# Performance work log

Measured on AMD Instinct MI355X. Metric: run time of the kernel, lower is better.

Reference implementation:

```python
import jax, jax.numpy as jnp
import numpy as np


def _gru(xs, w_ih, w_hh, b_ih, b_hh):
    """Batch-first torch-style GRU. xs: (B,T,I) -> (B,T,H)."""
    b, t, _ = xs.shape
    H = w_hh.shape[1]
    xp = xs @ w_ih.T + b_ih  # (B,T,3H): precomputed input projections

    def step(h, xp_t):
        gh = h @ w_hh.T + b_hh  # (B,3H)
        xr, xz, xn = xp_t[:, :H], xp_t[:, H:2 * H], xp_t[:, 2 * H:]
        hr, hz, hn = gh[:, :H], gh[:, H:2 * H], gh[:, 2 * H:]
        r = jax.nn.sigmoid(xr + hr)
        z = jax.nn.sigmoid(xz + hz)
        n = jnp.tanh(xn + r * hn)
        h_new = (1.0 - z) * n + z * h
        return h_new, h_new

    h0 = jnp.zeros((b, H), dtype=xs.dtype)
    _, hs = jax.lax.scan(step, h0, jnp.swapaxes(xp, 0, 1))  # (T,B,H)
    return jnp.swapaxes(hs, 0, 1)


def reference(x, gru_w_ih, gru_w_hh, gru_b_ih, gru_b_hh, filter_alpha, pc_w, pc_b, pat_re, pat_im):
    b, t, _ = x.shape
    xs = x[..., 0]  # (B,T)
    # quaternionic lift: (w,x,y,z) = (s, .1s, .01s, .001s)
    quat = jnp.stack([xs, 0.1 * xs, 0.01 * xs, 0.001 * xs], axis=-1)  # (B,T,4)
    evolved = _gru(quat, gru_w_ih, gru_w_hh, gru_b_ih, gru_b_hh)  # (B,T,4*dim)
    dim2 = evolved.shape[-1] // 2
    ev = evolved.reshape(b, t, dim2, 2)
    ec = jax.lax.complex(ev[..., 0], ev[..., 1])  # (B,T,2*dim) complex64
    fd = jnp.fft.fft(ec, axis=1)
    kmag = jnp.abs(fd) + 1e-10
    pf = filter_alpha[0] * jnp.arctan(jnp.log(kmag))  # phase filter
    filtered = fd * jax.lax.complex(jnp.cos(pf), jnp.sin(pf))
    ft = jnp.fft.ifft(filtered, axis=1).real  # (B,T,2*dim) float32
    coh = ft.reshape(b, t, -1) @ pc_w.T + pc_b  # (B,T,dim)
    # interference logits: |<x_t, pattern_j>|^2, computed only for batch 0
    # (faithful to original; x_t is real so vdot conjugation is a no-op)
    x0 = coh[0]  # (T,dim)
    zr = x0 @ pat_re.T  # (T,V)
    zi = x0 @ pat_im.T  # (T,V)
    logits0 = zr * zr + zi * zi
    return logits0[None]  # (1,T,V)


def setup_inputs() -> dict:
    key = jax.random.key(0)
    ks = jax.random.split(key, 10)
    dim, T, V = 128, 4096, 32000
    H = dim * 4
    return {
        "x": jax.random.normal(ks[0], (1, T, 1), jnp.float32),
        "gru_w_ih": jax.random.normal(ks[1], (3 * H, 4), jnp.float32) * 0.05,
        "gru_w_hh": jax.random.normal(ks[2], (3 * H, H), jnp.float32) * 0.05,
        "gru_b_ih": jax.random.normal(ks[3], (3 * H,), jnp.float32) * 0.05,
        "gru_b_hh": jax.random.normal(ks[4], (3 * H,), jnp.float32) * 0.05,
        "filter_alpha": jnp.ones((1,), jnp.float32) * 1.5,
        "pc_w": jax.random.normal(ks[5], (dim, 2 * dim), jnp.float32) * 0.05,
        "pc_b": jax.random.normal(ks[6], (dim,), jnp.float32) * 0.05,
        "pat_re": jax.random.normal(ks[7], (V, dim), jnp.float32) * 0.1,
        "pat_im": jax.random.normal(ks[8], (V, dim), jnp.float32) * 0.1,
    }
```

## Files before the change

kernel.cpp:

```cpp
#include <hip/hip_runtime.h>

#define T_STEPS 4096
#define HID     512
#define NCH     256
#define DIM     128
#define VOCAB   32000
#define GRU_WGS 32

__global__ __launch_bounds__(256) void gru_kernel(
    const float* __restrict__ x,
    const float* __restrict__ w_ih,
    const float* __restrict__ w_hh,
    const float* __restrict__ b_ih,
    const float* __restrict__ b_hh,
    unsigned long long* hg,
    float* __restrict__ evolved)
{
  __shared__ float hs[HID];
  const int tid  = threadIdx.x;
  const int wave = tid >> 6;
  const int lane = tid & 63;
  const int team = lane >> 4;
  const int p    = lane & 15;
  const int pr   = p & 7;
  const int j    = blockIdx.x * 16 + wave * 4 + team;
  const int k0   = p * 32;

  float4 w[3][8];
#pragma unroll
  for (int d = 0; d < 3; ++d) {
    const float4* wr = reinterpret_cast<const float4*>(w_hh + (size_t)(d * HID + j) * HID);
#pragma unroll
    for (int qq = 0; qq < 8; ++qq) {
      const int r = (qq + pr) & 7;
      w[d][qq] = wr[p * 8 + r];
    }
  }
  float c3[3], bi3[3], bh3[3];
#pragma unroll
  for (int d = 0; d < 3; ++d) {
    int r = d * HID + j;
    c3[d]  = w_ih[r*4+0] + 0.1f*w_ih[r*4+1] + 0.01f*w_ih[r*4+2] + 0.001f*w_ih[r*4+3];
    bi3[d] = b_ih[r];
    bh3[d] = b_hh[r];
  }

  float hprev = 0.0f;
  for (int s = 1; s <= T_STEPS; ++s) {
    const int rb = (s - 1) & 1;
    const int wb = s & 1;
    const unsigned int want = (unsigned int)(s - 1);
    const unsigned long long* rs = hg + rb * HID;

    const float xt = x[s - 1];

    unsigned long long vA, vB;
    for (;;) {
      vA = __hip_atomic_load(rs + 2 * tid,     __ATOMIC_RELAXED, __HIP_MEMORY_SCOPE_AGENT);
      vB = __hip_atomic_load(rs + 2 * tid + 1, __ATOMIC_RELAXED, __HIP_MEMORY_SCOPE_AGENT);
      const bool ok = ((unsigned int)(vA >> 32) == want) &
                      ((unsigned int)(vB >> 32) == want);
      if (__syncthreads_and(ok)) break;
    }
    hs[2 * tid]     = __uint_as_float((unsigned int)vA);
    hs[2 * tid + 1] = __uint_as_float((unsigned int)vB);
    __syncthreads();

    float a0 = 0.f, a1 = 0.f, a2 = 0.f;
#pragma unroll
    for (int qq = 0; qq < 8; ++qq) {
      const int r = (qq + pr) & 7;
      const float4 h4 = *reinterpret_cast<const float4*>(&hs[k0 + 4 * r]);
      a0 = fmaf(w[0][qq].x, h4.x, a0);
      a0 = fmaf(w[0][qq].y, h4.y, a0);
      a0 = fmaf(w[0][qq].z, h4.z, a0);
      a0 = fmaf(w[0][qq].w, h4.w, a0);
      a1 = fmaf(w[1][qq].x, h4.x, a1);
      a1 = fmaf(w[1][qq].y, h4.y, a1);
      a1 = fmaf(w[1][qq].z, h4.z, a1);
      a1 = fmaf(w[1][qq].w, h4.w, a1);
      a2 = fmaf(w[2][qq].x, h4.x, a2);
      a2 = fmaf(w[2][qq].y, h4.y, a2);
      a2 = fmaf(w[2][qq].z, h4.z, a2);
      a2 = fmaf(w[2][qq].w, h4.w, a2);
    }
#pragma unroll
    for (int m = 8; m >= 1; m >>= 1) {
      a0 += __shfl_xor(a0, m);
      a1 += __shfl_xor(a1, m);
      a2 += __shfl_xor(a2, m);
    }

    if (p == 0) {
      const float rg = 1.0f / (1.0f + expf(-(fmaf(xt, c3[0], bi3[0]) + a0 + bh3[0])));
      const float zg = 1.0f / (1.0f + expf(-(fmaf(xt, c3[1], bi3[1]) + a1 + bh3[1])));
      const float ng = tanhf(fmaf(xt, c3[2], bi3[2]) + rg * (a2 + bh3[2]));
      const float hn = (1.0f - zg) * ng + zg * hprev;
      hprev = hn;
      const unsigned long long pk =
          ((unsigned long long)(unsigned int)s << 32) | (unsigned long long)__float_as_uint(hn);
      __hip_atomic_store(hg + wb * HID + j, pk, __ATOMIC_RELAXED, __HIP_MEMORY_SCOPE_AGENT);
      evolved[(size_t)(s - 1) * HID + j] = hn;
    }
  }
}

__device__ __forceinline__ void fft4096(float2* buf, int tid)
{
  for (int st = 0; st < 12; ++st) {
    const int half = 1 << st;
    const int len  = 2 << st;
    const float ang0 = -6.283185307179586f / (float)len;
    for (int i = tid; i < 2048; i += 256) {
      const int blk = i >> st;
      const int pos = i & (half - 1);
      const int idx = blk * len + pos;
      float sn, cs;
      sincosf(ang0 * (float)pos, &sn, &cs);
      const float2 u = buf[idx];
      const float2 v = buf[idx + half];
      const float tr = v.x * cs - v.y * sn;
      const float ti = v.x * sn + v.y * cs;
      buf[idx]        = make_float2(u.x + tr, u.y + ti);
      buf[idx + half] = make_float2(u.x - tr, u.y - ti);
    }
    __syncthreads();
  }
}

__global__ __launch_bounds__(256) void fft_kernel(
    const float* __restrict__ evolved,
    const float* __restrict__ alpha_p,
    float* __restrict__ ft)
{
  __shared__ float2 buf[4096];
  const int tid = threadIdx.x;
  const int c = blockIdx.x;
  const float alpha = alpha_p[0];

  for (int t = tid; t < 4096; t += 256) {
    const int r = __brev((unsigned)t) >> 20;
    buf[r] = make_float2(evolved[(size_t)t * HID + 2 * c],
                         evolved[(size_t)t * HID + 2 * c + 1]);
  }
  __syncthreads();
  fft4096(buf, tid);

  for (int t = tid; t < 4096; t += 256) {
    float2 v = buf[t];
    const float km = sqrtf(v.x * v.x + v.y * v.y) + 1e-10f;
    const float pf = alpha * atanf(logf(km));
    float sn, cs;
    sincosf(pf, &sn, &cs);
    const float rr = v.x * cs - v.y * sn;
    const float ii = v.x * sn + v.y * cs;
    buf[t] = make_float2(rr, -ii);
  }
  __syncthreads();
  for (int t = tid; t < 4096; t += 256) {
    const int r = __brev((unsigned)t) >> 20;
    if (r > t) { float2 tmp = buf[t]; buf[t] = buf[r]; buf[r] = tmp; }
  }
  __syncthreads();
  fft4096(buf, tid);

  const float inv = 1.0f / 4096.0f;
  for (int t = tid; t < 4096; t += 256) {
    ft[(size_t)t * NCH + c] = buf[t].x * inv;
  }
}

__global__ __launch_bounds__(256) void coh_kernel(
    const float* __restrict__ ft,
    const float* __restrict__ pcw,
    const float* __restrict__ pcb,
    float* __restrict__ x0)
{
  __shared__ float wT[64][132];
  __shared__ float fT[64][68];
  const int tid = threadIdx.x;
  const int rg = tid >> 4;
  const int cg = tid & 15;
  const int t0 = blockIdx.x * 64;
  float acc[4][8];
#pragma unroll
  for (int i = 0; i < 4; ++i)
#pragma unroll
    for (int jj = 0; jj < 8; ++jj) acc[i][jj] = 0.f;

  for (int kt = 0; kt < 256; kt += 64) {
    __syncthreads();
    for (int u = tid; u < 64 * DIM; u += 256) {
      const int col = u >> 6, kk = u & 63;
      wT[kk][col] = pcw[col * 256 + kt + kk];
    }
    for (int u = tid; u < 64 * 64; u += 256) {
      const int row = u >> 6, kk = u & 63;
      fT[kk][row] = ft[(size_t)(t0 + row) * NCH + kt + kk];
    }
    __syncthreads();
#pragma unroll 4
    for (int k = 0; k < 64; ++k) {
      const float4 a  = *(const float4*)&fT[k][rg * 4];
      const float4 w0 = *(const float4*)&wT[k][cg * 8];
      const float4 w1 = *(const float4*)&wT[k][cg * 8 + 4];
      const float av[4] = {a.x, a.y, a.z, a.w};
      const float wv[8] = {w0.x, w0.y, w0.z, w0.w, w1.x, w1.y, w1.z, w1.w};
#pragma unroll
      for (int i = 0; i < 4; ++i)
#pragma unroll
        for (int jj = 0; jj < 8; ++jj)
          acc[i][jj] = fmaf(av[i], wv[jj], acc[i][jj]);
    }
  }
#pragma unroll
  for (int i = 0; i < 4; ++i) {
    const int t = t0 + rg * 4 + i;
#pragma unroll
    for (int jj = 0; jj < 8; ++jj)
      x0[(size_t)t * DIM + cg * 8 + jj] = acc[i][jj] + pcb[cg * 8 + jj];
  }
}

__global__ __launch_bounds__(256) void logits_kernel(
    const float* __restrict__ x0,
    const float* __restrict__ patre,
    const float* __restrict__ patim,
    float* __restrict__ out)
{
  __shared__ float aT[32][68];
  __shared__ float brT[32][132];
  __shared__ float biT[32][132];
  const int tid = threadIdx.x;
  const int tx = tid & 31;
  const int ty = tid >> 5;
  const int m0 = blockIdx.y * 64;
  const int n0 = blockIdx.x * 128;
  float accr[8][4], acci[8][4];
#pragma unroll
  for (int i = 0; i < 8; ++i)
#pragma unroll
    for (int jj = 0; jj < 4; ++jj) { accr[i][jj] = 0.f; acci[i][jj] = 0.f; }

  for (int kt = 0; kt < 128; kt += 32) {
    __syncthreads();
    for (int u = tid; u < 64 * 32; u += 256) {
      const int mm = u >> 5, kk = u & 31;
      aT[kk][mm] = x0[(size_t)(m0 + mm) * DIM + kt + kk];
    }
    for (int u = tid; u < 128 * 32; u += 256) {
      const int nn = u >> 5, kk = u & 31;
      brT[kk][nn] = patre[(size_t)(n0 + nn) * DIM + kt + kk];
      biT[kk][nn] = patim[(size_t)(n0 + nn) * DIM + kt + kk];
    }
    __syncthreads();
#pragma unroll 4
    for (int k = 0; k < 32; ++k) {
      const float4 q0 = *(const float4*)&aT[k][ty * 8];
      const float4 q1 = *(const float4*)&aT[k][ty * 8 + 4];
      const float4 br = *(const float4*)&brT[k][tx * 4];
      const float4 bi = *(const float4*)&biT[k][tx * 4];
      const float av[8]  = {q0.x, q0.y, q0.z, q0.w, q1.x, q1.y, q1.z, q1.w};
      const float brv[4] = {br.x, br.y, br.z, br.w};
      const float biv[4] = {bi.x, bi.y, bi.z, bi.w};
#pragma unroll
      for (int i = 0; i < 8; ++i)
#pragma unroll
        for (int jj = 0; jj < 4; ++jj) {
          accr[i][jj] = fmaf(av[i], brv[jj], accr[i][jj]);
          acci[i][jj] = fmaf(av[i], biv[jj], acci[i][jj]);
        }
    }
  }
#pragma unroll
  for (int i = 0; i < 8; ++i) {
    const size_t m = (size_t)(m0 + ty * 8 + i);
    float4 o;
    o.x = accr[i][0] * accr[i][0] + acci[i][0] * acci[i][0];
    o.y = accr[i][1] * accr[i][1] + acci[i][1] * acci[i][1];
    o.z = accr[i][2] * accr[i][2] + acci[i][2] * acci[i][2];
    o.w = accr[i][3] * accr[i][3] + acci[i][3] * acci[i][3];
    *(float4*)&out[m * VOCAB + n0 + tx * 4] = o;
  }
}

extern "C" void kernel_launch(void* const* d_in, const int* in_sizes, int n_in,
                              void* d_out, int out_size, void* d_ws, size_t ws_size,
                              hipStream_t stream)
{
  const float* x     = (const float*)d_in[0];
  const float* w_ih  = (const float*)d_in[1];
  const float* w_hh  = (const float*)d_in[2];
  const float* b_ih  = (const float*)d_in[3];
  const float* b_hh  = (const float*)d_in[4];
  const float* alpha = (const float*)d_in[5];
  const float* pc_w  = (const float*)d_in[6];
  const float* pc_b  = (const float*)d_in[7];
  const float* patre = (const float*)d_in[8];
  const float* patim = (const float*)d_in[9];

  float* out = (float*)d_out;
  float* evolved = out;
  float* ft      = out + 4194304;

  unsigned long long* hg = (unsigned long long*)d_ws;
  float* x0 = (float*)((char*)d_ws + 8192);

  hipMemsetAsync(d_ws, 0, 8192, stream);

  gru_kernel<<<GRU_WGS, 256, 0, stream>>>(x, w_ih, w_hh, b_ih, b_hh, hg, evolved);
  fft_kernel<<<256, 256, 0, stream>>>(evolved, alpha, ft);
  coh_kernel<<<64, 256, 0, stream>>>(ft, pc_w, pc_b, x0);
  logits_kernel<<<dim3(250, 64), 256, 0, stream>>>(x0, patre, patim, out);
}
```

Measured before the change: 11.56 ms.

## Speed up GRU step and FFT with DPP reductions, fast math, twiddle table

```diff
diff --git a/kernel.cpp b/kernel.cpp
--- a/kernel.cpp
+++ b/kernel.cpp
@@ -6,6 +6,30 @@
 #define DIM     128
 #define VOCAB   32000
 #define GRU_WGS 32
+
+__device__ __forceinline__ float fast_sigmoid(float x) {
+  x = fminf(fmaxf(x, -30.f), 30.f);
+  const float e = __expf(-x);
+  return __fdividef(1.f, 1.f + e);
+}
+__device__ __forceinline__ float fast_tanh(float x) {
+  x = fminf(fmaxf(x, -15.f), 15.f);
+  const float e = __expf(2.f * x);
+  return __fdividef(e - 1.f, e + 1.f);
+}
+
+template <int CTRL>
+__device__ __forceinline__ float dpp_add(float v) {
+  const int s = __builtin_amdgcn_update_dpp(0, __float_as_int(v), CTRL, 0xF, 0xF, true);
+  return v + __int_as_float(s);
+}
+__device__ __forceinline__ float red16(float v) {
+  v = dpp_add<0xB1>(v);
+  v = dpp_add<0x4E>(v);
+  v = dpp_add<0x124>(v);
+  v = dpp_add<0x128>(v);
+  return v;
+}
 
 __global__ __launch_bounds__(256) void gru_kernel(
     const float* __restrict__ x,
@@ -17,6 +41,7 @@
     float* __restrict__ evolved)
 {
   __shared__ float hs[HID];
+  __shared__ float xl[T_STEPS];
   const int tid  = threadIdx.x;
   const int wave = tid >> 6;
   const int lane = tid & 63;
@@ -26,6 +51,12 @@
   const int j    = blockIdx.x * 16 + wave * 4 + team;
   const int k0   = p * 32;
 
+  {
+    const float4* x4 = reinterpret_cast<const float4*>(x);
+    float4* xl4 = reinterpret_cast<float4*>(xl);
+    for (int u = tid; u < T_STEPS / 4; u += 256) xl4[u] = x4[u];
+  }
+
   float4 w[3][8];
 #pragma unroll
   for (int d = 0; d < 3; ++d) {
@@ -44,6 +75,7 @@
     bi3[d] = b_ih[r];
     bh3[d] = b_hh[r];
   }
+  __syncthreads();
 
   float hprev = 0.0f;
   for (int s = 1; s <= T_STEPS; ++s) {
@@ -52,15 +84,20 @@
     const unsigned int want = (unsigned int)(s - 1);
     const unsigned long long* rs = hg + rb * HID;
 
-    const float xt = x[s - 1];
+    const float xt = xl[s - 1];
 
     unsigned long long vA, vB;
+    vA = __hip_atomic_load(rs + 2 * tid,     __ATOMIC_RELAXED, __HIP_MEMORY_SCOPE_AGENT);
+    vB = __hip_atomic_load(rs + 2 * tid + 1, __ATOMIC_RELAXED, __HIP_MEMORY_SCOPE_AGENT);
     for (;;) {
-      vA = __hip_atomic_load(rs + 2 * tid,     __ATOMIC_RELAXED, __HIP_MEMORY_SCOPE_AGENT);
-      vB = __hip_atomic_load(rs + 2 * tid + 1, __ATOMIC_RELAXED, __HIP_MEMORY_SCOPE_AGENT);
       const bool ok = ((unsigned int)(vA >> 32) == want) &
                       ((unsigned int)(vB >> 32) == want);
+      const unsigned long long nA =
+          __hip_atomic_load(rs + 2 * tid,     __ATOMIC_RELAXED, __HIP_MEMORY_SCOPE_AGENT);
+      const unsigned long long nB =
+          __hip_atomic_load(rs + 2 * tid + 1, __ATOMIC_RELAXED, __HIP_MEMORY_SCOPE_AGENT);
       if (__syncthreads_and(ok)) break;
+      vA = nA; vB = nB;
     }
     hs[2 * tid]     = __uint_as_float((unsigned int)vA);
     hs[2 * tid + 1] = __uint_as_float((unsigned int)vB);
@@ -84,17 +121,13 @@
       a2 = fmaf(w[2][qq].z, h4.z, a2);
       a2 = fmaf(w[2][qq].w, h4.w, a2);
     }
-#pragma unroll
-    for (int m = 8; m >= 1; m >>= 1) {
-      a0 += __shfl_xor(a0, m);
-      a1 += __shfl_xor(a1, m);
-      a2 += __shfl_xor(a2, m);
-    }
+
+    a0 = red16(a0); a1 = red16(a1); a2 = red16(a2);
 
     if (p == 0) {
-      const float rg = 1.0f / (1.0f + expf(-(fmaf(xt, c3[0], bi3[0]) + a0 + bh3[0])));
-      const float zg = 1.0f / (1.0f + expf(-(fmaf(xt, c3[1], bi3[1]) + a1 + bh3[1])));
-      const float ng = tanhf(fmaf(xt, c3[2], bi3[2]) + rg * (a2 + bh3[2]));
+      const float rg = fast_sigmoid(fmaf(xt, c3[0], bi3[0]) + a0 + bh3[0]);
+      const float zg = fast_sigmoid(fmaf(xt, c3[1], bi3[1]) + a1 + bh3[1]);
+      const float ng = fast_tanh(fmaf(xt, c3[2], bi3[2]) + rg * (a2 + bh3[2]));
       const float hn = (1.0f - zg) * ng + zg * hprev;
       hprev = hn;
       const unsigned long long pk =
@@ -105,22 +138,20 @@
   }
 }
 
-__device__ __forceinline__ void fft4096(float2* buf, int tid)
+__device__ __forceinline__ void fft4096(float2* buf, const float2* tw, int tid)
 {
   for (int st = 0; st < 12; ++st) {
     const int half = 1 << st;
-    const int len  = 2 << st;
-    const float ang0 = -6.283185307179586f / (float)len;
+    const int sh = 11 - st;
     for (int i = tid; i < 2048; i += 256) {
       const int blk = i >> st;
       const int pos = i & (half - 1);
-      const int idx = blk * len + pos;
-      float sn, cs;
-      sincosf(ang0 * (float)pos, &sn, &cs);
+      const int idx = blk * (2 << st) + pos;
+      const float2 t = tw[pos << sh];
       const float2 u = buf[idx];
       const float2 v = buf[idx + half];
-      const float tr = v.x * cs - v.y * sn;
-      const float ti = v.x * sn + v.y * cs;
+      const float tr = v.x * t.x - v.y * t.y;
+      const float ti = v.x * t.y + v.y * t.x;
       buf[idx]        = make_float2(u.x + tr, u.y + ti);
       buf[idx + half] = make_float2(u.x - tr, u.y - ti);
     }
@@ -134,9 +165,16 @@
     float* __restrict__ ft)
 {
   __shared__ float2 buf[4096];
+  __shared__ float2 tw[2048];
   const int tid = threadIdx.x;
   const int c = blockIdx.x;
   const float alpha = alpha_p[0];
+
+  for (int k = tid; k < 2048; k += 256) {
+    float sn, cs;
+    sincosf(-6.283185307179586f * (float)k / 4096.0f, &sn, &cs);
+    tw[k] = make_float2(cs, sn);
+  }
 
   for (int t = tid; t < 4096; t += 256) {
     const int r = __brev((unsigned)t) >> 20;
@@ -144,7 +182,7 @@
                          evolved[(size_t)t * HID + 2 * c + 1]);
   }
   __syncthreads();
-  fft4096(buf, tid);
+  fft4096(buf, tw, tid);
 
   for (int t = tid; t < 4096; t += 256) {
     float2 v = buf[t];
@@ -162,7 +200,7 @@
     if (r > t) { float2 tmp = buf[t]; buf[t] = buf[r]; buf[r] = tmp; }
   }
   __syncthreads();
-  fft4096(buf, tid);
+  fft4096(buf, tw, tid);
 
   const float inv = 1.0f / 4096.0f;
   for (int t = tid; t < 4096; t += 256) {
@@ -304,7 +342,7 @@
   float* ft      = out + 4194304;
 
   unsigned long long* hg = (unsigned long long*)d_ws;
-  float* x0 = (float*)((char*)d_ws + 8192);
+  float* x0 = (float*)((char*)d_ws + 16384);
 
   hipMemsetAsync(d_ws, 0, 8192, stream);
 
```

New measurement: 10.05 ms, median of 2. 13.1% less time.
